# Kernel tuning notes

Measured on AMD Instinct MI355X. Metric: run time of the kernel, lower is better.

Reference implementation:

```python
import jax, jax.numpy as jnp
import numpy as np

P = 1024
D_FF = 4096
TGT = 4096
SRC = 4096


def _ln(x, g, b, eps=1e-5):
    mu = jnp.mean(x, axis=-1, keepdims=True)
    var = jnp.mean((x - mu) ** 2, axis=-1, keepdims=True)
    return (x - mu) / jnp.sqrt(var + eps) * g + b


def setup_inputs() -> dict:
    key = jax.random.key(0)
    ks = jax.random.split(key, 32)
    s = 1.0 / np.sqrt(P)
    sf = 1.0 / np.sqrt(D_FF)
    d = {
        "Y": jax.random.normal(ks[0], (TGT, P), jnp.float32),
        "Xp": jax.random.normal(ks[1], (SRC, P), jnp.float32),
        # self-attn projections (Linear: y = x @ W + b, W stored [in, out])
        "wq1": jax.random.uniform(ks[2], (P, P), jnp.float32, -s, s),
        "bq1": jnp.zeros((P,), jnp.float32),
        "wk1": jax.random.uniform(ks[3], (P, P), jnp.float32, -s, s),
        "bk1": jnp.zeros((P,), jnp.float32),
        "wv1": jax.random.uniform(ks[4], (P, P), jnp.float32, -s, s),
        "bv1": jnp.zeros((P,), jnp.float32),
        "w0": jax.random.uniform(ks[5], (P, P), jnp.float32, -s, s),
        "b0": jnp.zeros((P,), jnp.float32),
        "g1": jnp.ones((P,), jnp.float32),
        "be1": jnp.zeros((P,), jnp.float32),
        # cross-attn projections
        "wq2": jax.random.uniform(ks[6], (P, P), jnp.float32, -s, s),
        "bq2": jnp.zeros((P,), jnp.float32),
        "wk2": jax.random.uniform(ks[7], (P, P), jnp.float32, -s, s),
        "bk2": jnp.zeros((P,), jnp.float32),
        "wv2": jax.random.uniform(ks[8], (P, P), jnp.float32, -s, s),
        "bv2": jnp.zeros((P,), jnp.float32),
        "w1": jax.random.uniform(ks[9], (P, P), jnp.float32, -s, s),
        "b1": jnp.zeros((P,), jnp.float32),
        "g2": jnp.ones((P,), jnp.float32),
        "be2": jnp.zeros((P,), jnp.float32),
        # FFN
        "w2": jax.random.uniform(ks[10], (P, D_FF), jnp.float32, -s, s),
        "b2": jnp.zeros((D_FF,), jnp.float32),
        "w3": jax.random.uniform(ks[11], (D_FF, P), jnp.float32, -sf, sf),
        "b3": jnp.zeros((P,), jnp.float32),
        "g3": jnp.ones((P,), jnp.float32),
        "be3": jnp.zeros((P,), jnp.float32),
    }
    return d


def reference(Y, Xp, wq1, bq1, wk1, bk1, wv1, bv1, w0, b0, g1, be1,
              wq2, bq2, wk2, bk2, wv2, bv2, w1, b1, g2, be2,
              w2, b2, w3, b3, g3, be3):
    m = Y.shape[0]
    scale = 1.0 / jnp.sqrt(jnp.asarray(P, Y.dtype))
    # --- masked self-attention on Y ---
    Q = Y @ wq1 + bq1            # [m, p]
    K = Y @ wk1 + bk1
    V = Y @ wv1 + bv1
    S = (Q @ K.T) * scale        # [m, m]
    causal = jnp.tril(jnp.ones((m, m), bool))
    S = jnp.where(causal, S, jnp.asarray(-1e9, S.dtype))
    A = jax.nn.softmax(S, axis=-1)
    T1 = (A @ V) @ w0 + b0
    U1 = _ln(Y + T1, g1, be1)
    # --- cross-attention with encoder output Xp ---
    Q = U1 @ wq2 + bq2           # [m, p]
    K = Xp @ wk2 + bk2           # [n, p]
    V = Xp @ wv2 + bv2
    S = (Q @ K.T) * scale        # [m, n]
    A = jax.nn.softmax(S, axis=-1)
    T2 = (A @ V) @ w1 + b1
    U2 = _ln(U1 + T2, g2, be2)
    # --- position-wise FFN ---
    Z = jax.nn.relu(U2 @ w2 + b2) @ w3 + b3
    U3 = _ln(U2 + Z, g3, be3)
    return U3
```

## Files before the change

### kernel.cpp

```cpp
#include <hip/hip_runtime.h>
#include <hip/hip_bf16.h>

typedef __bf16 bf16x8 __attribute__((ext_vector_type(8)));
typedef __bf16 bf16x4 __attribute__((ext_vector_type(4)));
typedef float f32x4 __attribute__((ext_vector_type(4)));

#define AS1P(p) ((__attribute__((address_space(1))) void*)(void*)(p))
#define AS3P(p) ((__attribute__((address_space(3))) void*)(p))

__global__ __launch_bounds__(256, 3) void gemm_bt(
    const __hip_bfloat16* __restrict__ A, int lda,
    const __hip_bfloat16* __restrict__ Bt, int ldb,
    int M, int N, int K, int ldc,
    const float* __restrict__ bias, int bias_mode,
    float scale,
    const float* __restrict__ residual,
    int relu, int causal_skip, int trapezoid, int ksplit,
    float* __restrict__ Cf, __hip_bfloat16* __restrict__ Cb,
    int nsplit1, const __hip_bfloat16* __restrict__ A2,
    const __hip_bfloat16* __restrict__ Bt2, int ldb2, int ldc2,
    const float* __restrict__ bias2, __hip_bfloat16* __restrict__ Cb2)
{
    int nb = blockIdx.x;
    int mb = blockIdx.y;
    {
        const int gx = gridDim.x, gy = gridDim.y;
        if ((gx & 3) == 0 && (gy & 1) == 0) {
            const int id = mb * gx + nb;
            const int X  = id & 7;
            const int L  = id >> 3;
            const int rn = gx >> 2, rm = gy >> 1;
            const int nb_l = L / rm, mb_l = L - nb_l * rm;
            nb = (X & 3) * rn + nb_l;
            mb = (X >> 2) * rm + mb_l;
        }
    }
    if (nsplit1 && nb >= nsplit1) {
        A = A2; Bt = Bt2; ldb = ldb2; ldc = ldc2; bias = bias2;
        Cb = Cb2; Cf = nullptr; residual = nullptr;
        nb -= nsplit1;
    }
    const int m_base = mb * 128;
    const int n_base = nb * 128;
    if (causal_skip && (n_base > m_base + 127)) return;
    int Kend = K;
    if (trapezoid) { int kl = m_base + 128; Kend = kl < K ? kl : K; }
    int kb = 0, ke = Kend;
    if (ksplit) {
        kb = blockIdx.z * ksplit;
        int k2 = kb + ksplit; ke = k2 < Kend ? k2 : Kend;
        if (kb >= ke) return;
        Cb += (size_t)blockIdx.z * M * ldc;
        Cf = nullptr;
    }
    const int nt = (ke - kb) >> 5;

    __shared__ __align__(16) __hip_bfloat16 Lds[3][8192];

    const int tid  = threadIdx.x;
    const int lane = tid & 63;
    const int wave = tid >> 6;
    const int wm = (wave >> 1) * 64;
    const int wn = (wave & 1) * 64;

    f32x4 acc[4][4];
#pragma unroll
    for (int i = 0; i < 4; ++i)
#pragma unroll
        for (int j = 0; j < 4; ++j) acc[i][j] = f32x4{0.f, 0.f, 0.f, 0.f};

    const bool isA = wave < 2;
    const __hip_bfloat16* G = isA ? (A + (size_t)m_base * lda) : (Bt + (size_t)n_base * ldb);
    const int ldg = isA ? lda : ldb;
    const int q0 = (wave & 1) * 4;
    const int rsub = lane >> 2;
    const int cx   = (lane & 3) ^ ((lane >> 3) & 3);
    const size_t grow = (size_t)(q0 * 16 + rsub) * ldg + (size_t)cx * 8 + kb;
    const int ldsoff = (isA ? 0 : 4096) + q0 * 512;

    const int lrow = lane & 15;
    const int cph  = ((lane >> 4) ^ ((lrow >> 1) & 3)) * 8;

#define ISSUE_TILE(KT, STG)                                                      \
    {                                                                            \
        const __hip_bfloat16* g = G + grow + (size_t)(KT) * 32;                  \
        __hip_bfloat16* dst = &Lds[STG][ldsoff];                                 \
        _Pragma("unroll")                                                        \
        for (int q = 0; q < 4; ++q) {                                            \
            __builtin_amdgcn_global_load_lds(AS1P(g), AS3P(dst), 16, 0, 0);      \
            g += (size_t)16 * ldg; dst += 512;                                   \
        }                                                                        \
    }

    ISSUE_TILE(0, 0)
    if (nt > 1) ISSUE_TILE(1, 1)

    int cur = 0;
    for (int kt = 0; kt < nt; ++kt) {
        __builtin_amdgcn_sched_barrier(0);
        if (kt + 1 < nt) __builtin_amdgcn_s_waitcnt(0x0F74);
        else             __builtin_amdgcn_s_waitcnt(0x0F70);
        __builtin_amdgcn_sched_barrier(0);
        __builtin_amdgcn_s_barrier();
        __builtin_amdgcn_sched_barrier(0);
        if (kt + 2 < nt) {
            int s2 = cur + 2; if (s2 >= 3) s2 -= 3;
            ISSUE_TILE(kt + 2, s2)
        }

        bf16x8 af[4], bfv[4];
#pragma unroll
        for (int i = 0; i < 4; ++i)
            af[i] = *(const bf16x8*)&Lds[cur][(wm + i * 16 + lrow) * 32 + cph];
#pragma unroll
        for (int j = 0; j < 4; ++j)
            bfv[j] = *(const bf16x8*)&Lds[cur][4096 + (wn + j * 16 + lrow) * 32 + cph];
#pragma unroll
        for (int i = 0; i < 4; ++i)
#pragma unroll
            for (int j = 0; j < 4; ++j)
                acc[i][j] = __builtin_amdgcn_mfma_f32_16x16x32_bf16(af[i], bfv[j], acc[i][j], 0, 0, 0);

        cur = (cur + 1 == 3) ? 0 : cur + 1;
    }
#undef ISSUE_TILE

    const int r0 = (lane >> 4) * 4;
    const int c0 = lane & 15;
#pragma unroll
    for (int i = 0; i < 4; ++i) {
#pragma unroll
        for (int j = 0; j < 4; ++j) {
            const int col = n_base + wn + j * 16 + c0;
#pragma unroll
            for (int r = 0; r < 4; ++r) {
                const int row = m_base + wm + i * 16 + r0 + r;
                float v = acc[i][j][r] * scale;
                if (bias_mode == 1) v += bias[col];
                else if (bias_mode == 2) v += bias[row];
                if (relu) v = fmaxf(v, 0.f);
                const size_t idx = (size_t)row * ldc + col;
                if (residual) v += residual[idx];
                if (Cf) Cf[idx] = v;
                else    Cb[idx] = __float2bfloat16(v);
            }
        }
    }
}

__global__ __launch_bounds__(256, 2) void gemm_bt2(
    const __hip_bfloat16* __restrict__ A, int lda,
    const __hip_bfloat16* __restrict__ Bt, int ldb,
    int M, int N, int K, int ldc,
    const float* __restrict__ bias, int bias_mode,
    float scale,
    int relu, int causal_skip, int trapezoid, int ksplit,
    __hip_bfloat16* __restrict__ Cb)
{
    int nb = blockIdx.x;
    int mb = blockIdx.y;
    {
        const int gx = gridDim.x, gy = gridDim.y;
        if ((gx & 3) == 0 && (gy & 1) == 0) {
            const int id = mb * gx + nb;
            const int X  = id & 7;
            const int L  = id >> 3;
            const int rn = gx >> 2, rm = gy >> 1;
            const int nb_l = L / rm, mb_l = L - nb_l * rm;
            nb = (X & 3) * rn + nb_l;
            mb = (X >> 2) * rm + mb_l;
        }
    }
    const int m_base = mb * 256;
    const int n_base = nb * 128;
    if (causal_skip && (n_base > m_base + 255)) return;
    int Kend = K;
    if (trapezoid) { int kl = m_base + 256; Kend = kl < K ? kl : K; }
    int kb = 0, ke = Kend;
    if (ksplit) {
        kb = blockIdx.z * ksplit;
        int k2 = kb + ksplit; ke = k2 < Kend ? k2 : Kend;
        if (kb >= ke) return;
        Cb += (size_t)blockIdx.z * M * ldc;
    }
    const int nt = (ke - kb) >> 5;

    __shared__ __align__(16) __hip_bfloat16 Lds[3][12288];

    const int tid  = threadIdx.x;
    const int lane = tid & 63;
    const int wave = tid >> 6;
    const int wm = wave * 64;
    const int wtm = (wave >> 1) * 128;
    const int wtn = (wave & 1) * 64;

    f32x4 acc[8][4];
#pragma unroll
    for (int i = 0; i < 8; ++i)
#pragma unroll
        for (int j = 0; j < 4; ++j) acc[i][j] = f32x4{0.f, 0.f, 0.f, 0.f};

    const int rsub = lane >> 2;
    const int cx   = (lane & 3) ^ ((lane >> 3) & 3);
    const __hip_bfloat16* GA = A  + (size_t)(m_base + wave * 64) * lda + (size_t)rsub * lda + (size_t)cx * 8 + kb;
    const __hip_bfloat16* GB = Bt + (size_t)(n_base + wave * 32) * ldb + (size_t)rsub * ldb + (size_t)cx * 8 + kb;
    const int ldsA = wave * 2048;
    const int ldsB = 8192 + wave * 1024;

    const int lrow = lane & 15;
    const int cph  = ((lane >> 4) ^ ((lrow >> 1) & 3)) * 8;

#define ISSUE_TILE2(KT, STG)                                                     \
    {                                                                            \
        const size_t ko = (size_t)(KT) * 32;                                     \
        const __hip_bfloat16* ga = GA + ko;                                      \
        __hip_bfloat16* da = &Lds[STG][ldsA];                                    \
        _Pragma("unroll")                                                        \
        for (int q = 0; q < 4; ++q) {                                            \
            __builtin_amdgcn_global_load_lds(AS1P(ga), AS3P(da), 16, 0, 0);      \
            ga += (size_t)16 * lda; da += 512;                                   \
        }                                                                        \
        const __hip_bfloat16* gb = GB + ko;                                      \
        __hip_bfloat16* db = &Lds[STG][ldsB];                                    \
        _Pragma("unroll")                                                        \
        for (int q = 0; q < 2; ++q) {                                            \
            __builtin_amdgcn_global_load_lds(AS1P(gb), AS3P(db), 16, 0, 0);      \
            gb += (size_t)16 * ldb; db += 512;                                   \
        }                                                                        \
    }

    ISSUE_TILE2(0, 0)
    if (nt > 1) ISSUE_TILE2(1, 1)

    int cur = 0;
    for (int kt = 0; kt < nt; ++kt) {
        __builtin_amdgcn_sched_barrier(0);
        if (kt + 1 < nt) __builtin_amdgcn_s_waitcnt(0x0F76);
        else             __builtin_amdgcn_s_waitcnt(0x0F70);
        __builtin_amdgcn_sched_barrier(0);
        __builtin_amdgcn_s_barrier();
        __builtin_amdgcn_sched_barrier(0);
        if (kt + 2 < nt) {
            int s2 = cur + 2; if (s2 >= 3) s2 -= 3;
            ISSUE_TILE2(kt + 2, s2)
        }

        bf16x8 af[8], bfv[4];
#pragma unroll
        for (int i = 0; i < 8; ++i)
            af[i] = *(const bf16x8*)&Lds[cur][(wtm + i * 16 + lrow) * 32 + cph];
#pragma unroll
        for (int j = 0; j < 4; ++j)
            bfv[j] = *(const bf16x8*)&Lds[cur][8192 + (wtn + j * 16 + lrow) * 32 + cph];
#pragma unroll
        for (int i = 0; i < 8; ++i)
#pragma unroll
            for (int j = 0; j < 4; ++j)
                acc[i][j] = __builtin_amdgcn_mfma_f32_16x16x32_bf16(af[i], bfv[j], acc[i][j], 0, 0, 0);

        cur = (cur + 1 == 3) ? 0 : cur + 1;
    }
#undef ISSUE_TILE2

    const int r0 = (lane >> 4) * 4;
    const int c0 = lane & 15;
#pragma unroll
    for (int i = 0; i < 8; ++i) {
#pragma unroll
        for (int j = 0; j < 4; ++j) {
            const int col = n_base + wtn + j * 16 + c0;
#pragma unroll
            for (int r = 0; r < 4; ++r) {
                const int row = m_base + wtm + i * 16 + r0 + r;
                float v = acc[i][j][r] * scale;
                if (bias_mode == 1) v += bias[col];
                else if (bias_mode == 2) v += bias[row];
                if (relu) v = fmaxf(v, 0.f);
                Cb[(size_t)row * ldc + col] = __float2bfloat16(v);
            }
        }
    }
}

__global__ __launch_bounds__(256) void reduce_k_kernel(
    const __hip_bfloat16* __restrict__ Pb, int M, int N, int nsplit, int KC, int trapK,
    const float* __restrict__ bias, const float* __restrict__ residual,
    float* __restrict__ Cf, __hip_bfloat16* __restrict__ Cb)
{
    const int idx = blockIdx.x * 256 + threadIdx.x;
    const int nv = N >> 2;
    const int row = idx / nv;
    if (row >= M) return;
    const int c4 = (idx - row * nv) * 4;
    int nc = nsplit;
    if (trapK) {
        int kend = (row & ~255) + 256; if (kend > trapK) kend = trapK;
        nc = (kend + KC - 1) / KC;
    }
    float s0 = 0.f, s1 = 0.f, s2 = 0.f, s3 = 0.f;
    for (int c = 0; c < nc; ++c) {
        const bf16x4 p = *(const bf16x4*)(Pb + ((size_t)c * M + row) * N + c4);
        s0 += (float)p[0]; s1 += (float)p[1]; s2 += (float)p[2]; s3 += (float)p[3];
    }
    if (bias) {
        const f32x4 b = *(const f32x4*)(bias + c4);
        s0 += b[0]; s1 += b[1]; s2 += b[2]; s3 += b[3];
    }
    if (residual) {
        const f32x4 rv = *(const f32x4*)(residual + (size_t)row * N + c4);
        s0 += rv[0]; s1 += rv[1]; s2 += rv[2]; s3 += rv[3];
    }
    if (Cf) { f32x4 o = {s0, s1, s2, s3}; *(f32x4*)(Cf + (size_t)row * N + c4) = o; }
    else {
        bf16x4 o = { (__bf16)s0, (__bf16)s1, (__bf16)s2, (__bf16)s3 };
        *(bf16x4*)(Cb + (size_t)row * N + c4) = o;
    }
}

__global__ __launch_bounds__(256) void convert_bf16_kernel(
    const float* __restrict__ x, __hip_bfloat16* __restrict__ y, int n4)
{
    const int i = blockIdx.x * 256 + threadIdx.x;
    if (i >= n4) return;
    const float4 v = ((const float4*)x)[i];
    bf16x4 o = { (__bf16)v.x, (__bf16)v.y, (__bf16)v.z, (__bf16)v.w };
    *(bf16x4*)(y + (size_t)i * 4) = o;
}

__global__ __launch_bounds__(256) void transpose_convert_kernel(
    const float* __restrict__ W, __hip_bfloat16* __restrict__ Wt, int K, int N)
{
    __shared__ float t[32][33];
    const int k0 = blockIdx.y * 32;
    const int n0 = blockIdx.x * 32;
    const int tx = threadIdx.x;
    for (int i = threadIdx.y; i < 32; i += 8)
        t[i][tx] = W[(size_t)(k0 + i) * N + n0 + tx];
    __syncthreads();
    for (int i = threadIdx.y; i < 32; i += 8)
        Wt[(size_t)(n0 + i) * K + k0 + tx] = __float2bfloat16(t[tx][i]);
}

__global__ __launch_bounds__(256) void transpose_bf16_kernel(
    const __hip_bfloat16* __restrict__ src, int ls,
    __hip_bfloat16* __restrict__ dst, int ld)
{
    __shared__ __hip_bfloat16 t[32][33];
    const int r0 = blockIdx.y * 32;
    const int c0 = blockIdx.x * 32;
    const int tx = threadIdx.x;
    for (int i = threadIdx.y; i < 32; i += 8)
        t[i][tx] = src[(size_t)(r0 + i) * ls + c0 + tx];
    __syncthreads();
    for (int i = threadIdx.y; i < 32; i += 8)
        dst[(size_t)(c0 + i) * ld + r0 + tx] = t[tx][i];
}

__global__ __launch_bounds__(256) void softmax_kernel(
    const __hip_bfloat16* __restrict__ S, __hip_bfloat16* __restrict__ A, int N, int causal)
{
    __shared__ float sm[4];
    const int row = blockIdx.x;
    const int tid = threadIdx.x;
    const int limit = causal ? (row + 1) : N;
    const int zlimit = causal ? (((row & ~255) + 256) < N ? ((row & ~255) + 256) : N) : N;
    const __hip_bfloat16* Srow = S + (size_t)row * N;
    __hip_bfloat16* Arow = A + (size_t)row * N;
    const int nv = limit >> 2;

    float m = -3.0e38f;
    for (int v = tid; v < nv; v += 256) {
        const bf16x4 x = *(const bf16x4*)(Srow + (size_t)v * 4);
        m = fmaxf(m, fmaxf(fmaxf((float)x[0], (float)x[1]), fmaxf((float)x[2], (float)x[3])));
    }
    for (int j = (nv << 2) + tid; j < limit; j += 256) m = fmaxf(m, (float)Srow[j]);
#pragma unroll
    for (int o = 32; o; o >>= 1) m = fmaxf(m, __shfl_down(m, o));
    if ((tid & 63) == 0) sm[tid >> 6] = m;
    __syncthreads();
    m = fmaxf(fmaxf(sm[0], sm[1]), fmaxf(sm[2], sm[3]));
    __syncthreads();

    float s = 0.f;
    for (int v = tid; v < nv; v += 256) {
        const bf16x4 x = *(const bf16x4*)(Srow + (size_t)v * 4);
        s += __expf((float)x[0] - m) + __expf((float)x[1] - m)
           + __expf((float)x[2] - m) + __expf((float)x[3] - m);
    }
    for (int j = (nv << 2) + tid; j < limit; j += 256) s += __expf((float)Srow[j] - m);
#pragma unroll
    for (int o = 32; o; o >>= 1) s += __shfl_down(s, o);
    if ((tid & 63) == 0) sm[tid >> 6] = s;
    __syncthreads();
    s = sm[0] + sm[1] + sm[2] + sm[3];
    const float inv = 1.f / s;

    for (int v = tid; v < nv; v += 256) {
        const bf16x4 x = *(const bf16x4*)(Srow + (size_t)v * 4);
        bf16x4 o = { (__bf16)(__expf((float)x[0] - m) * inv), (__bf16)(__expf((float)x[1] - m) * inv),
                     (__bf16)(__expf((float)x[2] - m) * inv), (__bf16)(__expf((float)x[3] - m) * inv) };
        *(bf16x4*)(Arow + (size_t)v * 4) = o;
    }
    for (int j = (nv << 2) + tid; j < limit; j += 256)
        Arow[j] = __float2bfloat16(__expf((float)Srow[j] - m) * inv);
    const __hip_bfloat16 z = __float2bfloat16(0.f);
    for (int j = limit + tid; j < zlimit; j += 256) Arow[j] = z;
}

__global__ __launch_bounds__(256) void layernorm_kernel(
    const float* __restrict__ X, const float* __restrict__ g, const float* __restrict__ b,
    float* __restrict__ outF, __hip_bfloat16* __restrict__ outB)
{
    __shared__ float sm[8];
    const int row = blockIdx.x;
    const int tid = threadIdx.x;
    const float4 v = ((const float4*)(X + (size_t)row * 1024))[tid];
    float s  = v.x + v.y + v.z + v.w;
    float ss = v.x * v.x + v.y * v.y + v.z * v.z + v.w * v.w;
#pragma unroll
    for (int o = 32; o; o >>= 1) { s += __shfl_down(s, o); ss += __shfl_down(ss, o); }
    if ((tid & 63) == 0) { sm[tid >> 6] = s; sm[4 + (tid >> 6)] = ss; }
    __syncthreads();
    s  = sm[0] + sm[1] + sm[2] + sm[3];
    ss = sm[4] + sm[5] + sm[6] + sm[7];
    const float mu   = s * (1.f / 1024.f);
    const float var  = ss * (1.f / 1024.f) - mu * mu;
    const float rstd = rsqrtf(var + 1e-5f);
    const float4 gv = ((const float4*)g)[tid];
    const float4 bv = ((const float4*)b)[tid];
    float4 o;
    o.x = (v.x - mu) * rstd * gv.x + bv.x;
    o.y = (v.y - mu) * rstd * gv.y + bv.y;
    o.z = (v.z - mu) * rstd * gv.z + bv.z;
    o.w = (v.w - mu) * rstd * gv.w + bv.w;
    ((float4*)(outF + (size_t)row * 1024))[tid] = o;
    if (outB) {
        bf16x4 ob = { (__bf16)o.x, (__bf16)o.y, (__bf16)o.z, (__bf16)o.w };
        *(bf16x4*)(outB + (size_t)row * 1024 + (size_t)tid * 4) = ob;
    }
}

extern "C" void kernel_launch(void* const* d_in, const int* in_sizes, int n_in,
                              void* d_out, int out_size, void* d_ws, size_t ws_size,
                              hipStream_t stream)
{
    const int M = 4096, Pd = 1024, DFF = 4096, NS = 4096;
    const size_t MB = 1024 * 1024;

    const float* Y   = (const float*)d_in[0];
    const float* Xp  = (const float*)d_in[1];
    const float* wq1 = (const float*)d_in[2];  const float* bq1 = (const float*)d_in[3];
    const float* wk1 = (const float*)d_in[4];  const float* bk1 = (const float*)d_in[5];
    const float* wv1 = (const float*)d_in[6];  const float* bv1 = (const float*)d_in[7];
    const float* w0  = (const float*)d_in[8];  const float* b0  = (const float*)d_in[9];
    const float* g1  = (const float*)d_in[10]; const float* be1 = (const float*)d_in[11];
    const float* wq2 = (const float*)d_in[12]; const float* bq2 = (const float*)d_in[13];
    const float* wk2 = (const float*)d_in[14]; const float* bk2 = (const float*)d_in[15];
    const float* wv2 = (const float*)d_in[16]; const float* bv2 = (const float*)d_in[17];
    const float* w1  = (const float*)d_in[18]; const float* b1  = (const float*)d_in[19];
    const float* g2  = (const float*)d_in[20]; const float* be2 = (const float*)d_in[21];
    const float* w2  = (const float*)d_in[22]; const float* b2  = (const float*)d_in[23];
    const float* w3  = (const float*)d_in[24]; const float* b3  = (const float*)d_in[25];
    const float* g3  = (const float*)d_in[26]; const float* be3 = (const float*)d_in[27];

    char* ws = (char*)d_ws;
    __hip_bfloat16* Ybf   = (__hip_bfloat16*)(ws + 0 * MB);
    __hip_bfloat16* Ubf   = (__hip_bfloat16*)(ws + 0 * MB);
    __hip_bfloat16* Xpbf  = (__hip_bfloat16*)(ws + 8 * MB);
    __hip_bfloat16* AVbf  = (__hip_bfloat16*)(ws + 8 * MB);
    __hip_bfloat16* Qbf   = (__hip_bfloat16*)(ws + 8 * MB);
    __hip_bfloat16* wqkv1t= (__hip_bfloat16*)(ws + 16 * MB);
    __hip_bfloat16* w0t   = (__hip_bfloat16*)(ws + 22 * MB);
    __hip_bfloat16* wq2t  = (__hip_bfloat16*)(ws + 24 * MB);
    __hip_bfloat16* wkv2t = (__hip_bfloat16*)(ws + 26 * MB);
    __hip_bfloat16* w1t   = (__hip_bfloat16*)(ws + 30 * MB);
    __hip_bfloat16* w2t   = (__hip_bfloat16*)(ws + 32 * MB);
    __hip_bfloat16* w3t   = (__hip_bfloat16*)(ws + 40 * MB);
    float*          bqkv1 = (float*)(ws + 48 * MB);
    float*          bkv2  = (float*)(ws + 48 * MB + 512 * 1024);
    __hip_bfloat16* QKV1  = (__hip_bfloat16*)(ws + 49 * MB);
    __hip_bfloat16* KV2   = (__hip_bfloat16*)(ws + 73 * MB);
    __hip_bfloat16* Vt    = (__hip_bfloat16*)(ws + 89 * MB);
    __hip_bfloat16* Sb    = (__hip_bfloat16*)(ws + 97 * MB);
    __hip_bfloat16* Pb    = (__hip_bfloat16*)(ws + 97 * MB);
    __hip_bfloat16* Abf   = (__hip_bfloat16*)(ws + 161 * MB);
    float*          Xres  = (float*)(ws + 193 * MB);
    float*          Uf    = (float*)(ws + 209 * MB);
    float*          Out   = (float*)d_out;
    if (ws_size < 225 * MB) return;

    auto cvt = [&](const float* src, __hip_bfloat16* dst, int n) {
        convert_bf16_kernel<<<dim3(n / 1024), dim3(256), 0, stream>>>(src, dst, n / 4);
    };
    auto tconv = [&](const float* W, __hip_bfloat16* Wt, int K, int N) {
        transpose_convert_kernel<<<dim3(N / 32, K / 32), dim3(32, 8), 0, stream>>>(W, Wt, K, N);
    };
    auto tbf = [&](const __hip_bfloat16* src, int ls, __hip_bfloat16* dst, int ld, int R, int C) {
        transpose_bf16_kernel<<<dim3(C / 32, R / 32), dim3(32, 8), 0, stream>>>(src, ls, dst, ld);
    };
    auto gemm = [&](const __hip_bfloat16* A, int lda, const __hip_bfloat16* Bt, int ldb,
                    int Mm, int Nn, int Kk, int ldc,
                    const float* bias, int bmode, float scale, const float* res,
                    int relu, int causal, int trap, int ksplit,
                    float* Cf, __hip_bfloat16* Cb) {
        const int nz = ksplit ? (Kk + ksplit - 1) / ksplit : 1;
        gemm_bt<<<dim3(Nn / 128, Mm / 128, nz), dim3(256), 0, stream>>>(
            A, lda, Bt, ldb, Mm, Nn, Kk, ldc, bias, bmode, scale, res, relu, causal, trap, ksplit,
            Cf, Cb, 0, nullptr, nullptr, 0, 0, nullptr, nullptr);
    };
    auto gemm2 = [&](const __hip_bfloat16* A, int lda, const __hip_bfloat16* Bt, int ldb,
                     int Mm, int Nn, int Kk, int ldc,
                     const float* bias, int bmode, float scale,
                     int relu, int causal, int trap, int ksplit, __hip_bfloat16* Cb) {
        const int nz = ksplit ? (Kk + ksplit - 1) / ksplit : 1;
        gemm_bt2<<<dim3(Nn / 128, Mm / 256, nz), dim3(256), 0, stream>>>(
            A, lda, Bt, ldb, Mm, Nn, Kk, ldc, bias, bmode, scale, relu, causal, trap, ksplit, Cb);
    };
    auto reduce = [&](const __hip_bfloat16* P, int Mm, int Nn, int nsplit, int KC, int trapK,
                      const float* bias, const float* res, float* Cf, __hip_bfloat16* Cb) {
        reduce_k_kernel<<<dim3(Mm * Nn / 1024), dim3(256), 0, stream>>>(
            P, Mm, Nn, nsplit, KC, trapK, bias, res, Cf, Cb);
    };

    const float scl = 0.03125f;

    cvt(Y,  Ybf,  M * Pd);
    cvt(Xp, Xpbf, NS * Pd);
    tconv(wq1, wqkv1t,            Pd, Pd);
    tconv(wk1, wqkv1t + Pd * Pd,  Pd, Pd);
    tconv(wv1, wqkv1t + 2*Pd*Pd,  Pd, Pd);
    tconv(w0,  w0t,  Pd, Pd);
    tconv(wq2, wq2t, Pd, Pd);
    tconv(wk2, wkv2t,           Pd, Pd);
    tconv(wv2, wkv2t + Pd * Pd, Pd, Pd);
    tconv(w1,  w1t,  Pd, Pd);
    tconv(w2, w2t, Pd, DFF);
    tconv(w3, w3t, DFF, Pd);
    hipMemcpyAsync(bqkv1,            bq1, Pd * 4, hipMemcpyDeviceToDevice, stream);
    hipMemcpyAsync(bqkv1 + Pd,       bk1, Pd * 4, hipMemcpyDeviceToDevice, stream);
    hipMemcpyAsync(bqkv1 + 2 * Pd,   bv1, Pd * 4, hipMemcpyDeviceToDevice, stream);
    hipMemcpyAsync(bkv2,             bk2, Pd * 4, hipMemcpyDeviceToDevice, stream);
    hipMemcpyAsync(bkv2 + Pd,        bv2, Pd * 4, hipMemcpyDeviceToDevice, stream);

    gemm_bt<<<dim3(40, 32, 1), dim3(256), 0, stream>>>(
        Ybf, Pd, wqkv1t, Pd, M, 3072, Pd, 3072, bqkv1, 1, 1.f, nullptr, 0, 0, 0, 0,
        nullptr, QKV1,
        24, Xpbf, wkv2t, Pd, 2048, bkv2, KV2);

    tbf(QKV1 + 2048, 3072, Vt, M, M, Pd);
    gemm2(QKV1, 3072, QKV1 + 1024, 3072, M, M, Pd, M,
          nullptr, 0, scl, 0, 1, 0, 0, Sb);
    softmax_kernel<<<dim3(M), dim3(256), 0, stream>>>(Sb, Abf, M, 1);
    gemm2(Abf, M, Vt, M, M, Pd, M, Pd,
          nullptr, 0, 1.f, 0, 0, 1, 1024, Pb);
    reduce(Pb, M, Pd, 4, 1024, M, nullptr, nullptr, nullptr, AVbf);
    gemm(AVbf, Pd, w0t, Pd, M, Pd, Pd, Pd,
         nullptr, 0, 1.f, nullptr, 0, 0, 0, 512, nullptr, Pb);
    reduce(Pb, M, Pd, 2, 512, 0, b0, Y, Xres, nullptr);
    layernorm_kernel<<<dim3(M), dim3(256), 0, stream>>>(Xres, g1, be1, Uf, Ubf);

    gemm(Ubf, Pd, wq2t, Pd, M, Pd, Pd, Pd,
         nullptr, 0, 1.f, nullptr, 0, 0, 0, 512, nullptr, Pb);
    reduce(Pb, M, Pd, 2, 512, 0, bq2, nullptr, nullptr, Qbf);
    tbf(KV2 + 1024, 2048, Vt, NS, NS, Pd);
    gemm2(Qbf, Pd, KV2, 2048, M, NS, Pd, NS,
          nullptr, 0, scl, 0, 0, 0, 0, Sb);
    softmax_kernel<<<dim3(M), dim3(256), 0, stream>>>(Sb, Abf, NS, 0);
    gemm2(Abf, NS, Vt, NS, M, Pd, NS, Pd,
          nullptr, 0, 1.f, 0, 0, 0, 1024, Pb);
    reduce(Pb, M, Pd, 4, 1024, 0, nullptr, nullptr, nullptr, AVbf);
    gemm(AVbf, Pd, w1t, Pd, M, Pd, Pd, Pd,
         nullptr, 0, 1.f, nullptr, 0, 0, 0, 512, nullptr, Pb);
    reduce(Pb, M, Pd, 2, 512, 0, b1, Uf, Xres, nullptr);
    layernorm_kernel<<<dim3(M), dim3(256), 0, stream>>>(Xres, g2, be2, Uf, Ubf);

    gemm2(Ubf, Pd, w2t, Pd, M, DFF, Pd, DFF, b2, 1, 1.f, 1, 0, 0, 0, Abf);
    gemm2(Abf, DFF, w3t, DFF, M, Pd, DFF, Pd,
          nullptr, 0, 1.f, 0, 0, 0, 1024, Pb);
    reduce(Pb, M, Pd, 4, 1024, 0, b3, Uf, Xres, nullptr);
    layernorm_kernel<<<dim3(M), dim3(256), 0, stream>>>(Xres, g3, be3, Out, nullptr);
}
```

Baseline: 752.6 us.

## Fuse split-K reduce with layernorm, register-cache softmax, move QKV GEMM to gemm_bt2

Merges the split-K partial reduction, bias and residual add into the layernorm kernel. This removes the fp32 intermediate buffer and one launch per layer norm. The softmax now keeps each row in registers so S is read once instead of three times. The fused QKV/KV2 projection moves to the larger-tile gemm_bt2 kernel, which gains a dual-problem N-split mode. The reduce_ln step reads and writes Uf in place, which is safe only because each row is read fully before it is written.

```diff
diff --git a/kernel.cpp b/kernel.cpp
--- a/kernel.cpp
+++ b/kernel.cpp
@@ -155,7 +155,10 @@
     const float* __restrict__ bias, int bias_mode,
     float scale,
     int relu, int causal_skip, int trapezoid, int ksplit,
-    __hip_bfloat16* __restrict__ Cb)
+    __hip_bfloat16* __restrict__ Cb,
+    int nsplit1, const __hip_bfloat16* __restrict__ A2,
+    const __hip_bfloat16* __restrict__ Bt2, int ldb2, int ldc2,
+    const float* __restrict__ bias2, __hip_bfloat16* __restrict__ Cb2)
 {
     int nb = blockIdx.x;
     int mb = blockIdx.y;
@@ -171,6 +174,11 @@
             mb = (X >> 2) * rm + mb_l;
         }
     }
+    if (nsplit1 && nb >= nsplit1) {
+        A = A2; Bt = Bt2; ldb = ldb2; ldc = ldc2; bias = bias2;
+        Cb = Cb2;
+        nb -= nsplit1;
+    }
     const int m_base = mb * 256;
     const int n_base = nb * 128;
     if (causal_skip && (n_base > m_base + 255)) return;
@@ -190,7 +198,6 @@
     const int tid  = threadIdx.x;
     const int lane = tid & 63;
     const int wave = tid >> 6;
-    const int wm = wave * 64;
     const int wtm = (wave >> 1) * 128;
     const int wtn = (wave & 1) * 64;
 
@@ -317,106 +324,33 @@
     }
 }
 
-__global__ __launch_bounds__(256) void convert_bf16_kernel(
-    const float* __restrict__ x, __hip_bfloat16* __restrict__ y, int n4)
-{
-    const int i = blockIdx.x * 256 + threadIdx.x;
-    if (i >= n4) return;
-    const float4 v = ((const float4*)x)[i];
-    bf16x4 o = { (__bf16)v.x, (__bf16)v.y, (__bf16)v.z, (__bf16)v.w };
-    *(bf16x4*)(y + (size_t)i * 4) = o;
-}
-
-__global__ __launch_bounds__(256) void transpose_convert_kernel(
-    const float* __restrict__ W, __hip_bfloat16* __restrict__ Wt, int K, int N)
-{
-    __shared__ float t[32][33];
-    const int k0 = blockIdx.y * 32;
-    const int n0 = blockIdx.x * 32;
-    const int tx = threadIdx.x;
-    for (int i = threadIdx.y; i < 32; i += 8)
-        t[i][tx] = W[(size_t)(k0 + i) * N + n0 + tx];
-    __syncthreads();
-    for (int i = threadIdx.y; i < 32; i += 8)
-        Wt[(size_t)(n0 + i) * K + k0 + tx] = __float2bfloat16(t[tx][i]);
-}
-
-__global__ __launch_bounds__(256) void transpose_bf16_kernel(
-    const __hip_bfloat16* __restrict__ src, int ls,
-    __hip_bfloat16* __restrict__ dst, int ld)
-{
-    __shared__ __hip_bfloat16 t[32][33];
-    const int r0 = blockIdx.y * 32;
-    const int c0 = blockIdx.x * 32;
-    const int tx = threadIdx.x;
-    for (int i = threadIdx.y; i < 32; i += 8)
-        t[i][tx] = src[(size_t)(r0 + i) * ls + c0 + tx];
-    __syncthreads();
-    for (int i = threadIdx.y; i < 32; i += 8)
-        dst[(size_t)(c0 + i) * ld + r0 + tx] = t[tx][i];
-}
-
-__global__ __launch_bounds__(256) void softmax_kernel(
-    const __hip_bfloat16* __restrict__ S, __hip_bfloat16* __restrict__ A, int N, int causal)
-{
-    __shared__ float sm[4];
-    const int row = blockIdx.x;
-    const int tid = threadIdx.x;
-    const int limit = causal ? (row + 1) : N;
-    const int zlimit = causal ? (((row & ~255) + 256) < N ? ((row & ~255) + 256) : N) : N;
-    const __hip_bfloat16* Srow = S + (size_t)row * N;
-    __hip_bfloat16* Arow = A + (size_t)row * N;
-    const int nv = limit >> 2;
-
-    float m = -3.0e38f;
-    for (int v = tid; v < nv; v += 256) {
-        const bf16x4 x = *(const bf16x4*)(Srow + (size_t)v * 4);
-        m = fmaxf(m, fmaxf(fmaxf((float)x[0], (float)x[1]), fmaxf((float)x[2], (float)x[3])));
-    }
-    for (int j = (nv << 2) + tid; j < limit; j += 256) m = fmaxf(m, (float)Srow[j]);
-#pragma unroll
-    for (int o = 32; o; o >>= 1) m = fmaxf(m, __shfl_down(m, o));
-    if ((tid & 63) == 0) sm[tid >> 6] = m;
-    __syncthreads();
-    m = fmaxf(fmaxf(sm[0], sm[1]), fmaxf(sm[2], sm[3]));
-    __syncthreads();
-
-    float s = 0.f;
-    for (int v = tid; v < nv; v += 256) {
-        const bf16x4 x = *(const bf16x4*)(Srow + (size_t)v * 4);
-        s += __expf((float)x[0] - m) + __expf((float)x[1] - m)
-           + __expf((float)x[2] - m) + __expf((float)x[3] - m);
-    }
-    for (int j = (nv << 2) + tid; j < limit; j += 256) s += __expf((float)Srow[j] - m);
-#pragma unroll
-    for (int o = 32; o; o >>= 1) s += __shfl_down(s, o);
-    if ((tid & 63) == 0) sm[tid >> 6] = s;
-    __syncthreads();
-    s = sm[0] + sm[1] + sm[2] + sm[3];
-    const float inv = 1.f / s;
-
-    for (int v = tid; v < nv; v += 256) {
-        const bf16x4 x = *(const bf16x4*)(Srow + (size_t)v * 4);
-        bf16x4 o = { (__bf16)(__expf((float)x[0] - m) * inv), (__bf16)(__expf((float)x[1] - m) * inv),
-                     (__bf16)(__expf((float)x[2] - m) * inv), (__bf16)(__expf((float)x[3] - m) * inv) };
-        *(bf16x4*)(Arow + (size_t)v * 4) = o;
-    }
-    for (int j = (nv << 2) + tid; j < limit; j += 256)
-        Arow[j] = __float2bfloat16(__expf((float)Srow[j] - m) * inv);
-    const __hip_bfloat16 z = __float2bfloat16(0.f);
-    for (int j = limit + tid; j < zlimit; j += 256) Arow[j] = z;
-}
-
-__global__ __launch_bounds__(256) void layernorm_kernel(
-    const float* __restrict__ X, const float* __restrict__ g, const float* __restrict__ b,
+__global__ __launch_bounds__(256) void reduce_ln_kernel(
+    const __hip_bfloat16* __restrict__ Pb, int M, int nsplit,
+    const float* __restrict__ bias, const float* __restrict__ residual,
+    const float* __restrict__ g, const float* __restrict__ b,
     float* __restrict__ outF, __hip_bfloat16* __restrict__ outB)
 {
     __shared__ float sm[8];
     const int row = blockIdx.x;
     const int tid = threadIdx.x;
-    const float4 v = ((const float4*)(X + (size_t)row * 1024))[tid];
-    float s  = v.x + v.y + v.z + v.w;
-    float ss = v.x * v.x + v.y * v.y + v.z * v.z + v.w * v.w;
+    const int c4 = tid * 4;
+
+    float v0 = 0.f, v1 = 0.f, v2 = 0.f, v3 = 0.f;
+    for (int c = 0; c < nsplit; ++c) {
+        const bf16x4 p = *(const bf16x4*)(Pb + ((size_t)c * M + row) * 1024 + c4);
+        v0 += (float)p[0]; v1 += (float)p[1]; v2 += (float)p[2]; v3 += (float)p[3];
+    }
+    {
+        const f32x4 bv = *(const f32x4*)(bias + c4);
+        v0 += bv[0]; v1 += bv[1]; v2 += bv[2]; v3 += bv[3];
+    }
+    {
+        const f32x4 rv = *(const f32x4*)(residual + (size_t)row * 1024 + c4);
+        v0 += rv[0]; v1 += rv[1]; v2 += rv[2]; v3 += rv[3];
+    }
+
+    float s  = v0 + v1 + v2 + v3;
+    float ss = v0 * v0 + v1 * v1 + v2 * v2 + v3 * v3;
 #pragma unroll
     for (int o = 32; o; o >>= 1) { s += __shfl_down(s, o); ss += __shfl_down(ss, o); }
     if ((tid & 63) == 0) { sm[tid >> 6] = s; sm[4 + (tid >> 6)] = ss; }
@@ -429,14 +363,124 @@
     const float4 gv = ((const float4*)g)[tid];
     const float4 bv = ((const float4*)b)[tid];
     float4 o;
-    o.x = (v.x - mu) * rstd * gv.x + bv.x;
-    o.y = (v.y - mu) * rstd * gv.y + bv.y;
-    o.z = (v.z - mu) * rstd * gv.z + bv.z;
-    o.w = (v.w - mu) * rstd * gv.w + bv.w;
+    o.x = (v0 - mu) * rstd * gv.x + bv.x;
+    o.y = (v1 - mu) * rstd * gv.y + bv.y;
+    o.z = (v2 - mu) * rstd * gv.z + bv.z;
+    o.w = (v3 - mu) * rstd * gv.w + bv.w;
     ((float4*)(outF + (size_t)row * 1024))[tid] = o;
     if (outB) {
         bf16x4 ob = { (__bf16)o.x, (__bf16)o.y, (__bf16)o.z, (__bf16)o.w };
-        *(bf16x4*)(outB + (size_t)row * 1024 + (size_t)tid * 4) = ob;
+        *(bf16x4*)(outB + (size_t)row * 1024 + c4) = ob;
+    }
+}
+
+__global__ __launch_bounds__(256) void convert_bf16_kernel(
+    const float* __restrict__ x, __hip_bfloat16* __restrict__ y, int n4)
+{
+    const int i = blockIdx.x * 256 + threadIdx.x;
+    if (i >= n4) return;
+    const float4 v = ((const float4*)x)[i];
+    bf16x4 o = { (__bf16)v.x, (__bf16)v.y, (__bf16)v.z, (__bf16)v.w };
+    *(bf16x4*)(y + (size_t)i * 4) = o;
+}
+
+__global__ __launch_bounds__(256) void transpose_convert_kernel(
+    const float* __restrict__ W, __hip_bfloat16* __restrict__ Wt, int K, int N)
+{
+    __shared__ float t[32][33];
+    const int k0 = blockIdx.y * 32;
+    const int n0 = blockIdx.x * 32;
+    const int tx = threadIdx.x;
+    for (int i = threadIdx.y; i < 32; i += 8)
+        t[i][tx] = W[(size_t)(k0 + i) * N + n0 + tx];
+    __syncthreads();
+    for (int i = threadIdx.y; i < 32; i += 8)
+        Wt[(size_t)(n0 + i) * K + k0 + tx] = __float2bfloat16(t[tx][i]);
+}
+
+__global__ __launch_bounds__(256) void transpose_bf16_kernel(
+    const __hip_bfloat16* __restrict__ src, int ls,
+    __hip_bfloat16* __restrict__ dst, int ld)
+{
+    __shared__ __hip_bfloat16 t[32][33];
+    const int r0 = blockIdx.y * 32;
+    const int c0 = blockIdx.x * 32;
+    const int tx = threadIdx.x;
+    for (int i = threadIdx.y; i < 32; i += 8)
+        t[i][tx] = src[(size_t)(r0 + i) * ls + c0 + tx];
+    __syncthreads();
+    for (int i = threadIdx.y; i < 32; i += 8)
+        dst[(size_t)(c0 + i) * ld + r0 + tx] = t[tx][i];
+}
+
+__global__ __launch_bounds__(256) void softmax_kernel(
+    const __hip_bfloat16* __restrict__ S, __hip_bfloat16* __restrict__ A, int N, int causal)
+{
+    __shared__ float sm[4];
+    const int row = blockIdx.x;
+    const int tid = threadIdx.x;
+    const int limit = causal ? (row + 1) : N;
+    const int zl0 = (row & ~255) + 256;
+    const int zlimit = causal ? (zl0 < N ? zl0 : N) : N;
+    const __hip_bfloat16* Srow = S + (size_t)row * N;
+    __hip_bfloat16* Arow = A + (size_t)row * N;
+
+    float x[4][4];
+    float m = -3.0e38f;
+#pragma unroll
+    for (int p = 0; p < 4; ++p) {
+        const int cb = p * 1024 + tid * 4;
+        if (cb < limit) {
+            const bf16x4 xv = *(const bf16x4*)(Srow + cb);
+#pragma unroll
+            for (int e = 0; e < 4; ++e) {
+                const float f = (cb + e < limit) ? (float)xv[e] : -3.0e38f;
+                x[p][e] = f;
+                m = fmaxf(m, f);
+            }
+        } else {
+#pragma unroll
+            for (int e = 0; e < 4; ++e) x[p][e] = -3.0e38f;
+        }
+    }
+#pragma unroll
+    for (int o = 32; o; o >>= 1) m = fmaxf(m, __shfl_down(m, o));
+    if ((tid & 63) == 0) sm[tid >> 6] = m;
+    __syncthreads();
+    m = fmaxf(fmaxf(sm[0], sm[1]), fmaxf(sm[2], sm[3]));
+    __syncthreads();
+
+    float s = 0.f;
+#pragma unroll
+    for (int p = 0; p < 4; ++p) {
+        const int cb = p * 1024 + tid * 4;
+        if (cb < limit) {
+#pragma unroll
+            for (int e = 0; e < 4; ++e) {
+                const float ev = (cb + e < limit) ? __expf(x[p][e] - m) : 0.f;
+                x[p][e] = ev;
+                s += ev;
+            }
+        } else {
+#pragma unroll
+            for (int e = 0; e < 4; ++e) x[p][e] = 0.f;
+        }
+    }
+#pragma unroll
+    for (int o = 32; o; o >>= 1) s += __shfl_down(s, o);
+    if ((tid & 63) == 0) sm[tid >> 6] = s;
+    __syncthreads();
+    s = sm[0] + sm[1] + sm[2] + sm[3];
+    const float inv = 1.f / s;
+
+#pragma unroll
+    for (int p = 0; p < 4; ++p) {
+        const int cb = p * 1024 + tid * 4;
+        if (cb < zlimit) {
+            bf16x4 o = { (__bf16)(x[p][0] * inv), (__bf16)(x[p][1] * inv),
+                         (__bf16)(x[p][2] * inv), (__bf16)(x[p][3] * inv) };
+            *(bf16x4*)(Arow + cb) = o;
+        }
     }
 }
 
@@ -484,7 +528,6 @@
     __hip_bfloat16* Sb    = (__hip_bfloat16*)(ws + 97 * MB);
     __hip_bfloat16* Pb    = (__hip_bfloat16*)(ws + 97 * MB);
     __hip_bfloat16* Abf   = (__hip_bfloat16*)(ws + 161 * MB);
-    float*          Xres  = (float*)(ws + 193 * MB);
     float*          Uf    = (float*)(ws + 209 * MB);
     float*          Out   = (float*)d_out;
     if (ws_size < 225 * MB) return;
@@ -514,12 +557,20 @@
                      int relu, int causal, int trap, int ksplit, __hip_bfloat16* Cb) {
         const int nz = ksplit ? (Kk + ksplit - 1) / ksplit : 1;
         gemm_bt2<<<dim3(Nn / 128, Mm / 256, nz), dim3(256), 0, stream>>>(
-            A, lda, Bt, ldb, Mm, Nn, Kk, ldc, bias, bmode, scale, relu, causal, trap, ksplit, Cb);
+            A, lda, Bt, ldb, Mm, Nn, Kk, ldc, bias, bmode, scale, relu, causal, trap, ksplit, Cb,
+            0, nullptr, nullptr, 0, 0, nullptr, nullptr);
     };
     auto reduce = [&](const __hip_bfloat16* P, int Mm, int Nn, int nsplit, int KC, int trapK,
                       const float* bias, const float* res, float* Cf, __hip_bfloat16* Cb) {
         reduce_k_kernel<<<dim3(Mm * Nn / 1024), dim3(256), 0, stream>>>(
             P, Mm, Nn, nsplit, KC, trapK, bias, res, Cf, Cb);
+    };
+    auto reduce_ln = [&](const __hip_bfloat16* P, int nsplit,
+                         const float* bias, const float* res,
+                         const float* gg, const float* bb,
+                         float* outF, __hip_bfloat16* outB) {
+        reduce_ln_kernel<<<dim3(M), dim3(256), 0, stream>>>(
+            P, M, nsplit, bias, res, gg, bb, outF, outB);
     };
 
     const float scl = 0.03125f;
@@ -542,9 +593,9 @@
     hipMemcpyAsync(bkv2,             bk2, Pd * 4, hipMemcpyDeviceToDevice, stream);
     hipMemcpyAsync(bkv2 + Pd,        bv2, Pd * 4, hipMemcpyDeviceToDevice, stream);
 
-    gemm_bt<<<dim3(40, 32, 1), dim3(256), 0, stream>>>(
-        Ybf, Pd, wqkv1t, Pd, M, 3072, Pd, 3072, bqkv1, 1, 1.f, nullptr, 0, 0, 0, 0,
-        nullptr, QKV1,
+    gemm_bt2<<<dim3(40, 16, 1), dim3(256), 0, stream>>>(
+        Ybf, Pd, wqkv1t, Pd, M, 3072, Pd, 3072, bqkv1, 1, 1.f, 0, 0, 0, 0,
+        QKV1,
         24, Xpbf, wkv2t, Pd, 2048, bkv2, KV2);
 
     tbf(QKV1 + 2048, 3072, Vt, M, M, Pd);
@@ -556,8 +607,7 @@
     reduce(Pb, M, Pd, 4, 1024, M, nullptr, nullptr, nullptr, AVbf);
     gemm(AVbf, Pd, w0t, Pd, M, Pd, Pd, Pd,
          nullptr, 0, 1.f, nullptr, 0, 0, 0, 512, nullptr, Pb);
-    reduce(Pb, M, Pd, 2, 512, 0, b0, Y, Xres, nullptr);
-    layernorm_kernel<<<dim3(M), dim3(256), 0, stream>>>(Xres, g1, be1, Uf, Ubf);
+    reduce_ln(Pb, 2, b0, Y, g1, be1, Uf, Ubf);
 
     gemm(Ubf, Pd, wq2t, Pd, M, Pd, Pd, Pd,
          nullptr, 0, 1.f, nullptr, 0, 0, 0, 512, nullptr, Pb);
@@ -571,12 +621,10 @@
     reduce(Pb, M, Pd, 4, 1024, 0, nullptr, nullptr, nullptr, AVbf);
     gemm(AVbf, Pd, w1t, Pd, M, Pd, Pd, Pd,
          nullptr, 0, 1.f, nullptr, 0, 0, 0, 512, nullptr, Pb);
-    reduce(Pb, M, Pd, 2, 512, 0, b1, Uf, Xres, nullptr);
-    layernorm_kernel<<<dim3(M), dim3(256), 0, stream>>>(Xres, g2, be2, Uf, Ubf);
+    reduce_ln(Pb, 2, b1, Uf, g2, be2, Uf, Ubf);
 
     gemm2(Ubf, Pd, w2t, Pd, M, DFF, Pd, DFF, b2, 1, 1.f, 1, 0, 0, 0, Abf);
     gemm2(Abf, DFF, w3t, DFF, M, Pd, DFF, Pd,
           nullptr, 0, 1.f, 0, 0, 0, 1024, Pb);
-    reduce(Pb, M, Pd, 4, 1024, 0, b3, Uf, Xres, nullptr);
-    layernorm_kernel<<<dim3(M), dim3(256), 0, stream>>>(Xres, g3, be3, Out, nullptr);
-}
+    reduce_ln(Pb, 4, b3, Uf, g3, be3, Out, nullptr);
+}
```

Result: no change. 742.4 us (-1.3%).
